# Performance work log

Hardware: AMD Instinct MI355X
Metric: run time of the kernel (lower is better)

## Reference

```python
import jax, jax.numpy as jnp
import numpy as np

DATA_SZ = 1000   # number of timesteps, from source: data_sz = 1000
BATCH = 1024
DIM = 64
HIDDEN = 256


def setup_inputs() -> dict:
    key = jax.random.key(0)
    k0, k1, k2, k3, k4 = jax.random.split(key, 5)
    y0 = jax.random.normal(k0, (BATCH, DIM), dtype=jnp.float32)
    t = jnp.linspace(0.0, 15.0, DATA_SZ).astype(jnp.float32)
    W1 = jax.random.normal(k1, (DIM, HIDDEN), dtype=jnp.float32) * (1.0 / np.sqrt(DIM))
    b1 = jax.random.normal(k2, (HIDDEN,), dtype=jnp.float32) * 0.01
    W2 = jax.random.normal(k3, (HIDDEN, DIM), dtype=jnp.float32) * (1.0 / np.sqrt(HIDDEN))
    b2 = jax.random.normal(k4, (DIM,), dtype=jnp.float32) * 0.01
    return {"y0": y0, "t": t, "W1": W1, "b1": b1, "W2": W2, "b2": b2}


def reference(y0, t, W1, b1, W2, b2):
    # func: autonomous tanh-MLP vector field f(t, y) = tanh(y@W1+b1)@W2+b2
    def func(ti, y):
        return jnp.tanh(y @ W1 + b1) @ W2 + b2

    # solver: classic RK4 step returning dy (matches solver(func, t0, h, y0) -> dy)
    def rk4_dy(t0, h, y):
        half = h * 0.5
        k1 = func(t0, y)
        k2 = func(t0 + half, y + half * k1)
        k3 = func(t0 + half, y + half * k2)
        k4 = func(t0 + h, y + h * k3)
        return (h / 6.0) * (k1 + 2.0 * k2 + 2.0 * k3 + k4)

    ts = t[:-1]
    hs = t[1:] - t[:-1]

    def step(y, th):
        t0, h = th
        y1 = y + rk4_dy(t0, h, y)
        return y1, y1

    _, ys = jax.lax.scan(step, y0, (ts, hs))  # ys: [T-1, B, D]
    return jnp.concatenate([y0[None], ys], axis=0)  # [T, B, D]
```

## Files before the change

### kernel.cpp

```cpp
#include <hip/hip_runtime.h>


#define NB 1024
#define ND 64
#define NH 256
#define RPB 2
#define NBLK (NB / RPB)
#define NTHR 512

#define XB_OFF 0
#define AB_OFF 512
#define PART_OFF 1024
#define LDS_FL (PART_OFF + RPB * ND * 5)

#define R64(M) M(0) M(1) M(2) M(3) M(4) M(5) M(6) M(7) M(8) M(9) \
  M(10) M(11) M(12) M(13) M(14) M(15) M(16) M(17) M(18) M(19) \
  M(20) M(21) M(22) M(23) M(24) M(25) M(26) M(27) M(28) M(29) \
  M(30) M(31) M(32) M(33) M(34) M(35) M(36) M(37) M(38) M(39) \
  M(40) M(41) M(42) M(43) M(44) M(45) M(46) M(47) M(48) M(49) \
  M(50) M(51) M(52) M(53) M(54) M(55) M(56) M(57) M(58) M(59) \
  M(60) M(61) M(62) M(63)

#define Q16(M) M(0,0,1,2,3) M(1,4,5,6,7) M(2,8,9,10,11) M(3,12,13,14,15) \
  M(4,16,17,18,19) M(5,20,21,22,23) M(6,24,25,26,27) M(7,28,29,30,31) \
  M(8,32,33,34,35) M(9,36,37,38,39) M(10,40,41,42,43) M(11,44,45,46,47) \
  M(12,48,49,50,51) M(13,52,53,54,55) M(14,56,57,58,59) M(15,60,61,62,63)

__device__ __forceinline__ float fast_tanh(float x) {
    float e = __expf(2.0f * x);
    float r = __builtin_amdgcn_rcpf(e + 1.0f);
    return 1.0f - 2.0f * r;
}

#define BSYNC() do {                                             \
    asm volatile("s_waitcnt lgkmcnt(0)" ::: "memory");           \
    __builtin_amdgcn_s_barrier();                                \
    asm volatile("" ::: "memory");                               \
} while (0)

#define G1Q(q, i0, i1, i2, i3) {                                 \
    float4 xa_ = xq0[q]; float4 xb_ = xq1[q];                    \
    h0a = fmaf(w1_##i0, xa_.x, h0a); h0b = fmaf(w1_##i0, xb_.x, h0b); \
    h1a = fmaf(w1_##i1, xa_.y, h1a); h1b = fmaf(w1_##i1, xb_.y, h1b); \
    h0a = fmaf(w1_##i2, xa_.z, h0a); h0b = fmaf(w1_##i2, xb_.z, h0b); \
    h1a = fmaf(w1_##i3, xa_.w, h1a); h1b = fmaf(w1_##i3, xb_.w, h1b); \
}

#define G2Q(q, i0, i1, i2, i3) {                                 \
    float4 aa_ = aq0[q]; float4 ab_ = aq1[q];                    \
    p00 = fmaf(w2_##i0, aa_.x, p00); p10 = fmaf(w2_##i0, ab_.x, p10); \
    p01 = fmaf(w2_##i1, aa_.y, p01); p11 = fmaf(w2_##i1, ab_.y, p11); \
    p00 = fmaf(w2_##i2, aa_.z, p00); p10 = fmaf(w2_##i2, ab_.z, p10); \
    p01 = fmaf(w2_##i3, aa_.w, p01); p11 = fmaf(w2_##i3, ab_.w, p11); \
}

#define G1STAGE(X0, X1, K0, K1) do {                             \
    xbw[l]      = (X0);                                          \
    xbw[ND + l] = (X1);                                          \
    float h0a = b1l, h1a = 0.0f, h0b = b1l, h1b = 0.0f;          \
    Q16(G1Q)                                                     \
    abp[j]      = fast_tanh(h0a + h1a);                          \
    abp[NH + j] = fast_tanh(h0b + h1b);                          \
    BSYNC();                            \
    BSYNC();                     \
    { const float* pr = lds + PART_OFF + l * 5;                  \
      (K0) = ((pr[0] + pr[1]) + (pr[2] + pr[3])) + b2l;          \
      pr += 320;                                                 \
      (K1) = ((pr[0] + pr[1]) + (pr[2] + pr[3])) + b2l; }        \
} while (0)

__global__ __launch_bounds__(NTHR, 4)
void node_rk4_kernel(const float* __restrict__ y0,
                     const float* __restrict__ t,
                     const float* W1,
                     const float* b1,
                     const float* W2,
                     const float* b2,
                     float* __restrict__ out,
                     int nsteps)
{
    __shared__ float lds[LDS_FL];
    const int tid = threadIdx.x;
    const int w   = tid >> 6;
    const int l   = tid & 63;

    if (w < 4) {
        const int j = (w << 6) + l;
        const float b1l = b1[j];
        const float b2l = b2[l];
        #define DW1(i) float w1_##i;
        R64(DW1)
        #define LW1(i) w1_##i = W1[(i) * NH + j];
        R64(LW1)

        float* xbw = lds + XB_OFF + (w << 7);
        const float4* xq0 = (const float4*)xbw;
        const float4* xq1 = (const float4*)(xbw + ND);
        float* abp = lds + AB_OFF;

        const int row0 = blockIdx.x * RPB;
        float ya = y0[(row0 + 0) * ND + l];
        float yb = y0[(row0 + 1) * ND + l];
        if (w == 0) {
            out[(row0 + 0) * ND + l] = ya;
            out[(row0 + 1) * ND + l] = yb;
        }

        for (int s = 0; s < nsteps; ++s) {
            float dt  = t[s + 1] - t[s];
            float dt2 = 0.5f * dt;
            float k1a, k1b, k2a, k2b, k3a, k3b, k4a, k4b;
            G1STAGE(ya, yb, k1a, k1b);
            G1STAGE(fmaf(dt2, k1a, ya), fmaf(dt2, k1b, yb), k2a, k2b);
            G1STAGE(fmaf(dt2, k2a, ya), fmaf(dt2, k2b, yb), k3a, k3b);
            G1STAGE(fmaf(dt,  k3a, ya), fmaf(dt,  k3b, yb), k4a, k4b);
            float c6 = dt * (1.0f / 6.0f);
            ya = fmaf(c6, (k1a + k4a) + 2.0f * (k2a + k3a), ya);
            yb = fmaf(c6, (k1b + k4b) + 2.0f * (k2b + k3b), yb);
            if (w == 0) {
                size_t o = (size_t)(s + 1) * (NB * ND);
                out[o + (row0 + 0) * ND + l] = ya;
                out[o + (row0 + 1) * ND + l] = yb;
            }
        }
    } else {
        const int jj = w - 4;
        #define DW2(i) float w2_##i;
        R64(DW2)
        #define LW2(i) w2_##i = W2[((jj << 6) + (i)) * ND + l];
        R64(LW2)

        const float4* aq0 = (const float4*)(lds + AB_OFF + (jj << 6));
        const float4* aq1 = (const float4*)(lds + AB_OFF + NH + (jj << 6));
        float* pw = lds + PART_OFF;

        const int niter = 4 * nsteps;
        for (int it = 0; it < niter; ++it) {
            BSYNC();
            float p00 = 0.0f, p01 = 0.0f, p10 = 0.0f, p11 = 0.0f;
            Q16(G2Q)
            pw[0   + l * 5 + jj] = p00 + p01;
            pw[320 + l * 5 + jj] = p10 + p11;
            BSYNC();
        }
    }
}

extern "C" void kernel_launch(void* const* d_in, const int* in_sizes, int n_in,
                              void* d_out, int out_size, void* d_ws, size_t ws_size,
                              hipStream_t stream) {
    const float* y0 = (const float*)d_in[0];
    const float* t  = (const float*)d_in[1];
    const float* W1 = (const float*)d_in[2];
    const float* b1 = (const float*)d_in[3];
    const float* W2 = (const float*)d_in[4];
    const float* b2 = (const float*)d_in[5];
    float* out = (float*)d_out;
    int nsteps = in_sizes[1] - 1;
    hipLaunchKernelGGL(node_rk4_kernel, dim3(NBLK), dim3(NTHR), 0, stream,
                       y0, t, W1, b1, W2, b2, out, nsteps);
}
```

Measured before the change: 5.415 ms.

## Pipeline two rows across layer-1 and layer-2 warp groups with ping-pong buffers

Splits the two batch rows per block into independent chains A and B. Layer-1 waves work on one row while layer-2 waves work on the other, so the two warp groups overlap instead of idling in turn. Each half-stage now needs one barrier instead of the previous two, and LDS buffers are double-buffered per row. The cost is a more intricate barrier schedule whose correctness depends on the exact interleaving, and each group now does half the per-slot work with less ILP.

```diff
diff --git a/kernel.cpp b/kernel.cpp
--- a/kernel.cpp
+++ b/kernel.cpp
@@ -4,14 +4,12 @@
 #define NB 1024
 #define ND 64
 #define NH 256
-#define RPB 2
-#define NBLK (NB / RPB)
+#define NBLK 512
 #define NTHR 512
 
-#define XB_OFF 0
-#define AB_OFF 512
-#define PART_OFF 1024
-#define LDS_FL (PART_OFF + RPB * ND * 5)
+#define XBOF(C,W) (((C)<<8) + ((W)<<6))
+#define ABOF(C)   (512 + ((C)<<8))
+#define PTOF(C)   (1024 + (C)*320)
 
 #define R64(M) M(0) M(1) M(2) M(3) M(4) M(5) M(6) M(7) M(8) M(9) \
   M(10) M(11) M(12) M(13) M(14) M(15) M(16) M(17) M(18) M(19) \
@@ -38,37 +36,6 @@
     asm volatile("" ::: "memory");                               \
 } while (0)
 
-#define G1Q(q, i0, i1, i2, i3) {                                 \
-    float4 xa_ = xq0[q]; float4 xb_ = xq1[q];                    \
-    h0a = fmaf(w1_##i0, xa_.x, h0a); h0b = fmaf(w1_##i0, xb_.x, h0b); \
-    h1a = fmaf(w1_##i1, xa_.y, h1a); h1b = fmaf(w1_##i1, xb_.y, h1b); \
-    h0a = fmaf(w1_##i2, xa_.z, h0a); h0b = fmaf(w1_##i2, xb_.z, h0b); \
-    h1a = fmaf(w1_##i3, xa_.w, h1a); h1b = fmaf(w1_##i3, xb_.w, h1b); \
-}
-
-#define G2Q(q, i0, i1, i2, i3) {                                 \
-    float4 aa_ = aq0[q]; float4 ab_ = aq1[q];                    \
-    p00 = fmaf(w2_##i0, aa_.x, p00); p10 = fmaf(w2_##i0, ab_.x, p10); \
-    p01 = fmaf(w2_##i1, aa_.y, p01); p11 = fmaf(w2_##i1, ab_.y, p11); \
-    p00 = fmaf(w2_##i2, aa_.z, p00); p10 = fmaf(w2_##i2, ab_.z, p10); \
-    p01 = fmaf(w2_##i3, aa_.w, p01); p11 = fmaf(w2_##i3, ab_.w, p11); \
-}
-
-#define G1STAGE(X0, X1, K0, K1) do {                             \
-    xbw[l]      = (X0);                                          \
-    xbw[ND + l] = (X1);                                          \
-    float h0a = b1l, h1a = 0.0f, h0b = b1l, h1b = 0.0f;          \
-    Q16(G1Q)                                                     \
-    abp[j]      = fast_tanh(h0a + h1a);                          \
-    abp[NH + j] = fast_tanh(h0b + h1b);                          \
-    BSYNC();                            \
-    BSYNC();                     \
-    { const float* pr = lds + PART_OFF + l * 5;                  \
-      (K0) = ((pr[0] + pr[1]) + (pr[2] + pr[3])) + b2l;          \
-      pr += 320;                                                 \
-      (K1) = ((pr[0] + pr[1]) + (pr[2] + pr[3])) + b2l; }        \
-} while (0)
-
 __global__ __launch_bounds__(NTHR, 4)
 void node_rk4_kernel(const float* __restrict__ y0,
                      const float* __restrict__ t,
@@ -79,7 +46,7 @@
                      float* __restrict__ out,
                      int nsteps)
 {
-    __shared__ float lds[LDS_FL];
+    __shared__ float lds[1664];
     const int tid = threadIdx.x;
     const int w   = tid >> 6;
     const int l   = tid & 63;
@@ -93,35 +60,59 @@
         #define LW1(i) w1_##i = W1[(i) * NH + j];
         R64(LW1)
 
-        float* xbw = lds + XB_OFF + (w << 7);
-        const float4* xq0 = (const float4*)xbw;
-        const float4* xq1 = (const float4*)(xbw + ND);
-        float* abp = lds + AB_OFF;
+        float* xbwA = lds + XBOF(0, w);
+        float* xbwB = lds + XBOF(1, w);
+        const float4* xqA = (const float4*)xbwA;
+        const float4* xqB = (const float4*)xbwB;
+        float* abA = lds + ABOF(0) + (w << 6);
+        float* abB = lds + ABOF(1) + (w << 6);
+        const float* prA = lds + PTOF(0);
+        const float* prB = lds + PTOF(1);
 
-        const int row0 = blockIdx.x * RPB;
-        float ya = y0[(row0 + 0) * ND + l];
-        float yb = y0[(row0 + 1) * ND + l];
+        const int row0 = blockIdx.x * 2;
+        float yA = y0[(row0 + 0) * ND + l];
+        float yB = y0[(row0 + 1) * ND + l];
+        float kaA = 0.0f, kaB = 0.0f;
         if (w == 0) {
-            out[(row0 + 0) * ND + l] = ya;
-            out[(row0 + 1) * ND + l] = yb;
+            out[(size_t)(row0 + 0) * ND + l] = yA;
+            out[(size_t)(row0 + 1) * ND + l] = yB;
         }
+        float dt = 0.0f, dt2 = 0.0f, dt6 = 0.0f;
+        size_t obase = 0;
 
+#define G1Q(q,i0,i1,i2,i3) { float4 xv_ = xq_[q]; \
+    h0_ = fmaf(w1_##i0, xv_.x, h0_); h1_ = fmaf(w1_##i1, xv_.y, h1_); \
+    h0_ = fmaf(w1_##i2, xv_.z, h0_); h1_ = fmaf(w1_##i3, xv_.w, h1_); }
+
+#define G1SLOT(C, CI, ST) do {                                       \
+    float x_;                                                        \
+    if ((ST) == 0) { x_ = y##C; }                                    \
+    else {                                                           \
+      const float* pr_ = pr##C + l * 5;                              \
+      float kc_ = ((pr_[0] + pr_[1]) + (pr_[2] + pr_[3])) + b2l;     \
+      if ((ST)==1)      { ka##C  = kc_;       x_ = fmaf(dt2, kc_, y##C); } \
+      else if ((ST)==2) { ka##C += 2.0f*kc_;  x_ = fmaf(dt2, kc_, y##C); } \
+      else if ((ST)==3) { ka##C += 2.0f*kc_;  x_ = fmaf(dt,  kc_, y##C); } \
+      else { y##C = fmaf(dt6, ka##C + kc_, y##C); x_ = y##C;         \
+             if (w == 0) out[obase + (CI) * ND + l] = y##C; }        \
+    }                                                                \
+    xbw##C[l] = x_;                                                  \
+    asm volatile("s_waitcnt lgkmcnt(0)" ::: "memory");               \
+    const float4* xq_ = xq##C;                                       \
+    float h0_ = b1l, h1_ = 0.0f;                                     \
+    Q16(G1Q)                                                         \
+    ab##C[l] = fast_tanh(h0_ + h1_);                                 \
+} while (0)
+
+        G1SLOT(A, 0, 0); BSYNC();
+        G1SLOT(B, 1, 0); BSYNC();
         for (int s = 0; s < nsteps; ++s) {
-            float dt  = t[s + 1] - t[s];
-            float dt2 = 0.5f * dt;
-            float k1a, k1b, k2a, k2b, k3a, k3b, k4a, k4b;
-            G1STAGE(ya, yb, k1a, k1b);
-            G1STAGE(fmaf(dt2, k1a, ya), fmaf(dt2, k1b, yb), k2a, k2b);
-            G1STAGE(fmaf(dt2, k2a, ya), fmaf(dt2, k2b, yb), k3a, k3b);
-            G1STAGE(fmaf(dt,  k3a, ya), fmaf(dt,  k3b, yb), k4a, k4b);
-            float c6 = dt * (1.0f / 6.0f);
-            ya = fmaf(c6, (k1a + k4a) + 2.0f * (k2a + k3a), ya);
-            yb = fmaf(c6, (k1b + k4b) + 2.0f * (k2b + k3b), yb);
-            if (w == 0) {
-                size_t o = (size_t)(s + 1) * (NB * ND);
-                out[o + (row0 + 0) * ND + l] = ya;
-                out[o + (row0 + 1) * ND + l] = yb;
-            }
+            dt = t[s + 1] - t[s]; dt2 = 0.5f * dt; dt6 = dt * (1.0f / 6.0f);
+            obase = (size_t)(s + 1) * (NB * ND) + (size_t)row0 * ND;
+            G1SLOT(A, 0, 1); BSYNC();  G1SLOT(B, 1, 1); BSYNC();
+            G1SLOT(A, 0, 2); BSYNC();  G1SLOT(B, 1, 2); BSYNC();
+            G1SLOT(A, 0, 3); BSYNC();  G1SLOT(B, 1, 3); BSYNC();
+            G1SLOT(A, 0, 4); BSYNC();  G1SLOT(B, 1, 4); BSYNC();
         }
     } else {
         const int jj = w - 4;
@@ -130,18 +121,29 @@
         #define LW2(i) w2_##i = W2[((jj << 6) + (i)) * ND + l];
         R64(LW2)
 
-        const float4* aq0 = (const float4*)(lds + AB_OFF + (jj << 6));
-        const float4* aq1 = (const float4*)(lds + AB_OFF + NH + (jj << 6));
-        float* pw = lds + PART_OFF;
+        const float4* aqA = (const float4*)(lds + ABOF(0) + (jj << 6));
+        const float4* aqB = (const float4*)(lds + ABOF(1) + (jj << 6));
+        float* pwA = lds + PTOF(0);
+        float* pwB = lds + PTOF(1);
 
-        const int niter = 4 * nsteps;
-        for (int it = 0; it < niter; ++it) {
-            BSYNC();
-            float p00 = 0.0f, p01 = 0.0f, p10 = 0.0f, p11 = 0.0f;
-            Q16(G2Q)
-            pw[0   + l * 5 + jj] = p00 + p01;
-            pw[320 + l * 5 + jj] = p10 + p11;
-            BSYNC();
+#define G2Q(q,i0,i1,i2,i3) { float4 av_ = aq_[q]; \
+    p0_ = fmaf(w2_##i0, av_.x, p0_); p1_ = fmaf(w2_##i1, av_.y, p1_); \
+    p0_ = fmaf(w2_##i2, av_.z, p0_); p1_ = fmaf(w2_##i3, av_.w, p1_); }
+
+#define G2SLOT(C) do {                                               \
+    const float4* aq_ = aq##C;                                       \
+    float p0_ = 0.0f, p1_ = 0.0f;                                    \
+    Q16(G2Q)                                                         \
+    pw##C[l * 5 + jj] = p0_ + p1_;      \
+} while (0)
+
+        BSYNC();
+        G2SLOT(A); BSYNC();
+        for (int s = 0; s < nsteps; ++s) {
+            G2SLOT(B); BSYNC();  G2SLOT(A); BSYNC();
+            G2SLOT(B); BSYNC();  G2SLOT(A); BSYNC();
+            G2SLOT(B); BSYNC();  G2SLOT(A); BSYNC();
+            G2SLOT(B); BSYNC();  G2SLOT(A); BSYNC();
         }
     }
 }
```

Measured after the change: 4.674 ms. 13.7% less time.
